# Optimization experiments

Hardware: AMD Instinct MI355X
Metric: run time of the kernel (lower is better)

Reference implementation:

```python
import jax, jax.numpy as jnp
import numpy as np

N = 10000      # num nodes
E = 320000     # num edges
IN = 256       # in_dim
MP = 256       # mp_width
FL = 512       # fl_width
OUT = 64       # out_dim


def setup_inputs() -> dict:
    key = jax.random.key(0)
    ks = jax.random.split(key, 20)
    inp = {}
    inp["x"] = jax.random.normal(ks[0], (N, IN), dtype=jnp.float32)
    inp["edge_index"] = jax.random.randint(ks[1], (2, E), 0, N, dtype=jnp.int64)
    # iMP (frozen) linear layers: weight ~ N(0, 1) per nn.init.normal_(std=1.0)
    inp["mp_w0"] = jax.random.normal(ks[2], (IN, MP), dtype=jnp.float32)
    inp["mp_b0"] = jax.random.uniform(ks[3], (MP,), minval=-1.0, maxval=1.0) / np.sqrt(IN)
    inp["mp_w1"] = jax.random.normal(ks[4], (MP, MP), dtype=jnp.float32)
    inp["mp_b1"] = jax.random.uniform(ks[5], (MP,), minval=-1.0, maxval=1.0) / np.sqrt(MP)
    inp["mp_w2"] = jax.random.normal(ks[6], (MP, MP), dtype=jnp.float32)
    inp["mp_b2"] = jax.random.uniform(ks[7], (MP,), minval=-1.0, maxval=1.0) / np.sqrt(MP)
    # FC layers (torch default Linear init scale ~ 1/sqrt(fan_in))
    inp["fc_w0"] = jax.random.normal(ks[8], (MP, FL), dtype=jnp.float32) / np.sqrt(MP)
    inp["fc_b0"] = jnp.zeros((FL,), dtype=jnp.float32)
    inp["fc_w1"] = jax.random.normal(ks[9], (FL, FL), dtype=jnp.float32) / np.sqrt(FL)
    inp["fc_b1"] = jnp.zeros((FL,), dtype=jnp.float32)
    # injection projections
    inp["inj_w0"] = jax.random.normal(ks[10], (MP, FL), dtype=jnp.float32) / np.sqrt(MP)
    inp["inj_b0"] = jnp.zeros((FL,), dtype=jnp.float32)
    inp["inj_w1"] = jax.random.normal(ks[11], (MP, FL), dtype=jnp.float32) / np.sqrt(MP)
    inp["inj_b1"] = jnp.zeros((FL,), dtype=jnp.float32)
    inp["alpha"] = jnp.array(1.0, dtype=jnp.float32)
    inp["out_w"] = jax.random.normal(ks[12], (FL, OUT), dtype=jnp.float32) / np.sqrt(FL)
    inp["out_b"] = jnp.zeros((OUT,), dtype=jnp.float32)
    return inp


def _imp(x, w, b, row, col, deg_inv):
    # h = relu(W x); h /= deg; Ah = scatter_add over row of h[col]
    h = jax.nn.relu(x @ w + b) * deg_inv[:, None]      # [N, out]
    return jnp.zeros_like(h).at[row].add(h[col])       # gather + scatter-add


def reference(x, edge_index, mp_w0, mp_b0, mp_w1, mp_b1, mp_w2, mp_b2,
              fc_w0, fc_b0, fc_w1, fc_b1, inj_w0, inj_b0, inj_w1, inj_b1,
              alpha, out_w, out_b):
    row, col = edge_index[0], edge_index[1]
    deg = jax.ops.segment_sum(jnp.ones((E,), x.dtype), col, num_segments=N)
    # nodes with deg==0 never appear in col so clamping does not change output
    deg_inv = 1.0 / jnp.maximum(deg, 1.0)

    h = _imp(x, mp_w0, mp_b0, row, col, deg_inv)
    h = _imp(h, mp_w1, mp_b1, row, col, deg_inv)
    h = _imp(h, mp_w2, mp_b2, row, col, deg_inv)

    x_inject = h
    h = alpha * (jax.nn.relu(h) @ fc_w0 + fc_b0) + (x_inject @ inj_w0 + inj_b0)
    h = alpha * (jax.nn.relu(h) @ fc_w1 + fc_b1) + (x_inject @ inj_w1 + inj_b1)
    return h @ out_w + out_b
```

## Files before the change

### kernel.cpp

```cpp
#include <hip/hip_runtime.h>

#define N_NODES 10000
#define N_EDGES 320000
#define MPAD 10112
#define NBIN 10048
#define CHUNK 2048
#define NCH 157
#define CAP 128
#define PREP_BLOCKS 512
#define PREP_TOT 1148480L

typedef unsigned short u16;
typedef short bf16x8 __attribute__((ext_vector_type(8)));
typedef float f32x4 __attribute__((ext_vector_type(4)));

__device__ __forceinline__ u16 f2b(float f) {
  unsigned u = __builtin_bit_cast(unsigned, f);
  unsigned r = u + 0x7fffu + ((u >> 16) & 1u);
  return (u16)(r >> 16);
}
__device__ __forceinline__ unsigned pack2(float a, float b) {
  return (unsigned)f2b(a) | ((unsigned)f2b(b) << 16);
}
__device__ __forceinline__ float blo(unsigned u) { return __builtin_bit_cast(float, u << 16); }
__device__ __forceinline__ float bhi(unsigned u) { return __builtin_bit_cast(float, u & 0xffff0000u); }

struct PP {
  const float *x;
  const float *w0, *w1, *w2, *fcw0, *injw0, *fcw1, *injw1, *outw;
  const float *fcb0, *injb0, *fcb1, *injb1, *alpha, *outb;
  u16 *xb, *w0t, *w1t, *w2t, *wc1t, *wft;
  float *bias1, *bf;
};

__global__ __launch_bounds__(256) void edge_hist(const int* __restrict__ ei,
                                                 unsigned* __restrict__ histRC) {
  __shared__ unsigned sh[NBIN];
  const int tid = threadIdx.x, ch = blockIdx.x;
  for (int i = tid; i < NBIN; i += 256) sh[i] = 0;
  __syncthreads();
  const int e0 = ch * CHUNK;
#pragma unroll
  for (int j = 0; j < CHUNK; j += 256) {
    int e = e0 + j + tid;
    if (e < N_EDGES) {
      atomicAdd(&sh[ei[e]], 1u);
      atomicAdd(&sh[ei[N_EDGES + e]], 65536u);
    }
  }
  __syncthreads();
  for (int i = tid; i < NBIN; i += 256)
    histRC[(size_t)ch * NBIN + i] = sh[i];
}

__global__ __launch_bounds__(256) void prep(PP P) {
  const float alpha = P.alpha[0];
  const long stride = (long)PREP_BLOCKS * 256;
  for (long ii = (long)blockIdx.x * 256 + threadIdx.x; ii < PREP_TOT; ii += stride) {
    long i = ii;
    if (i < 640000L) {
      float4 v = ((const float4*)P.x)[i];
      uint2 o;
      o.x = pack2(v.x, v.y);
      o.y = pack2(v.z, v.w);
      *(uint2*)(P.xb + 4 * i) = o;
      continue;
    }
    i -= 640000L;
    if (i < 65536) { P.w0t[i] = f2b(P.w0[(i & 255) * 256 + (i >> 8)]); continue; }
    i -= 65536;
    if (i < 65536) { P.w1t[i] = f2b(P.w1[(i & 255) * 256 + (i >> 8)]); continue; }
    i -= 65536;
    if (i < 65536) { P.w2t[i] = f2b(P.w2[(i & 255) * 256 + (i >> 8)]); continue; }
    i -= 65536;
    if (i < 262144) {
      int n = (int)(i >> 9), k = (int)(i & 511);
      float v = (k < 256) ? alpha * P.fcw0[k * 512 + n] : P.injw0[(k - 256) * 512 + n];
      P.wc1t[i] = f2b(v); continue;
    }
    i -= 262144;
    if (i < 49152) {
      int n = (int)(i & 63), k = (int)(i >> 6);
      const float* fr = (k < 512) ? P.fcw1 + (size_t)k * 512
                                  : P.injw1 + (size_t)(k - 512) * 512;
      float a0 = 0.f, a1 = 0.f, a2 = 0.f, a3 = 0.f;
#pragma unroll 4
      for (int j = 0; j < 512; j += 4) {
        float4 f = *(const float4*)(fr + j);
        a0 += f.x * P.outw[(j + 0) * 64 + n];
        a1 += f.y * P.outw[(j + 1) * 64 + n];
        a2 += f.z * P.outw[(j + 2) * 64 + n];
        a3 += f.w * P.outw[(j + 3) * 64 + n];
      }
      float acc = (a0 + a1) + (a2 + a3);
      if (k < 512) acc *= alpha;
      P.wft[n * 768 + k] = f2b(acc);
      continue;
    }
    i -= 49152;
    if (i < 64) {
      float acc = P.outb[i];
#pragma unroll 8
      for (int j = 0; j < 512; ++j)
        acc += (alpha * P.fcb1[j] + P.injb1[j]) * P.outw[j * 64 + i];
      P.bf[i] = acc;
      continue;
    }
    i -= 64;
    if (i < 512) { P.bias1[i] = alpha * P.fcb0[i] + P.injb0[i]; continue; }
  }
}

__global__ __launch_bounds__(64) void col_scan(const unsigned* __restrict__ histRC,
                                               u16* __restrict__ chunkoff,
                                               int* __restrict__ cnt,
                                               float* __restrict__ deg_inv) {
  int r = blockIdx.x * 64 + threadIdx.x;
  if (r >= MPAD) return;
  if (r >= NBIN) { deg_inv[r] = 1.0f; return; }
  unsigned run = 0;
#pragma unroll 8
  for (int ch = 0; ch < NCH; ++ch) {
    chunkoff[(size_t)ch * NBIN + r] = (u16)(run & 0xffffu);
    run += histRC[(size_t)ch * NBIN + r];
  }
  int cr = (int)(run & 0xffffu);
  int dg = (int)(run >> 16);
  cnt[r] = cr;
  deg_inv[r] = 1.0f / (float)(dg > 1 ? dg : 1);
}

__global__ __launch_bounds__(256) void place_edges(const int* __restrict__ ei,
                                                   const u16* __restrict__ chunkoff,
                                                   int* __restrict__ csr) {
  __shared__ int cur[NBIN];
  const int ch = blockIdx.x, t = threadIdx.x;
  const u16* co = chunkoff + (size_t)ch * NBIN;
  for (int i = t; i < NBIN; i += 256) cur[i] = co[i];
  __syncthreads();
  const int e0 = ch * CHUNK;
#pragma unroll
  for (int j = 0; j < CHUNK; j += 256) {
    int e = e0 + j + t;
    if (e < N_EDGES) {
      int r = ei[e];
      int c = ei[N_EDGES + e];
      int rank = atomicAdd(&cur[r], 1);
      if (rank < CAP) csr[r * CAP + rank] = c;
    }
  }
}

template<int K, bool RELU, bool SCALE, bool F32OUT>
__global__ __launch_bounds__(128) void gemm64(
    const u16* __restrict__ A, int lda,
    const u16* __restrict__ Bt,
    const float* __restrict__ bias,
    const float* __restrict__ scale,
    u16* __restrict__ Cb, float* __restrict__ Cf, int ldc)
{
  __shared__ u16 As[64 * 72];
  __shared__ u16 Bs[64 * 72];
  const int tid = threadIdx.x;
  const int m0 = blockIdx.x * 64;
  const int n0 = blockIdx.y * 64;
  const int wave = tid >> 6;
  const int lane = tid & 63;
  const int wr = wave * 32;
  const int lm = lane & 15;
  const int koff = (lane >> 4) * 8;

  const int srow = tid >> 2;
  const int scol = (tid & 3) * 16;
  const u16* Ag0 = A + (size_t)(m0 + srow) * lda + scol;
  const u16* Ag1 = A + (size_t)(m0 + srow + 32) * lda + scol;
  const u16* Bg0 = Bt + (size_t)(n0 + srow) * K + scol;
  const u16* Bg1 = Bt + (size_t)(n0 + srow + 32) * K + scol;
  u16* Asw0 = &As[srow * 72 + scol];
  u16* Asw1 = &As[(srow + 32) * 72 + scol];
  u16* Bsw0 = &Bs[srow * 72 + scol];
  u16* Bsw1 = &Bs[(srow + 32) * 72 + scol];

  f32x4 acc[2][4] = {};

  int4 pa0 = *(const int4*)(Ag0),     pa1 = *(const int4*)(Ag0 + 8);
  int4 pa2 = *(const int4*)(Ag1),     pa3 = *(const int4*)(Ag1 + 8);
  int4 pb0 = *(const int4*)(Bg0),     pb1 = *(const int4*)(Bg0 + 8);
  int4 pb2 = *(const int4*)(Bg1),     pb3 = *(const int4*)(Bg1 + 8);

#pragma unroll
  for (int kb = 0; kb < K; kb += 64) {
    __syncthreads();
    *(int4*)Asw0 = pa0; *(int4*)(Asw0 + 8) = pa1;
    *(int4*)Asw1 = pa2; *(int4*)(Asw1 + 8) = pa3;
    *(int4*)Bsw0 = pb0; *(int4*)(Bsw0 + 8) = pb1;
    *(int4*)Bsw1 = pb2; *(int4*)(Bsw1 + 8) = pb3;
    __syncthreads();
    if (kb + 64 < K) {
      pa0 = *(const int4*)(Ag0 + kb + 64); pa1 = *(const int4*)(Ag0 + kb + 72);
      pa2 = *(const int4*)(Ag1 + kb + 64); pa3 = *(const int4*)(Ag1 + kb + 72);
      pb0 = *(const int4*)(Bg0 + kb + 64); pb1 = *(const int4*)(Bg0 + kb + 72);
      pb2 = *(const int4*)(Bg1 + kb + 64); pb3 = *(const int4*)(Bg1 + kb + 72);
    }
#pragma unroll
    for (int ks = 0; ks < 2; ++ks) {
      bf16x8 af[2], bf[4];
#pragma unroll
      for (int mi = 0; mi < 2; ++mi)
        af[mi] = *(const bf16x8*)&As[(wr + mi * 16 + lm) * 72 + ks * 32 + koff];
#pragma unroll
      for (int ni = 0; ni < 4; ++ni)
        bf[ni] = *(const bf16x8*)&Bs[(ni * 16 + lm) * 72 + ks * 32 + koff];
#pragma unroll
      for (int mi = 0; mi < 2; ++mi)
#pragma unroll
        for (int ni = 0; ni < 4; ++ni)
          acc[mi][ni] = __builtin_amdgcn_mfma_f32_16x16x32_bf16(af[mi], bf[ni], acc[mi][ni], 0, 0, 0);
    }
  }

  const int q4 = (lane >> 4) * 4;
#pragma unroll
  for (int mi = 0; mi < 2; ++mi) {
#pragma unroll
    for (int ni = 0; ni < 4; ++ni) {
      const int gc = n0 + ni * 16 + lm;
      const float bv = bias[gc];
#pragma unroll
      for (int r = 0; r < 4; ++r) {
        const int gr = m0 + wr + mi * 16 + q4 + r;
        float v = acc[mi][ni][r] + bv;
        if (RELU) v = fmaxf(v, 0.f);
        if (SCALE) v *= scale[gr];
        if (F32OUT) {
          if (gr < N_NODES) Cf[(size_t)gr * ldc + gc] = v;
        } else {
          Cb[(size_t)gr * ldc + gc] = f2b(v);
        }
      }
    }
  }
}

__global__ __launch_bounds__(256) void aggregate(
    const u16* __restrict__ tmp, const int* __restrict__ cnt,
    const int* __restrict__ csr, u16* __restrict__ out0,
    u16* __restrict__ A1, u16* __restrict__ A2, int mode)
{
  const int wv = threadIdx.x >> 6;
  const int lane = threadIdx.x & 63;
  const int r = blockIdx.x * 4 + wv;
  const int half = lane >> 5;
  const int q = lane & 31;
  const int beg = r * CAP, end = beg + cnt[r];
  const size_t feat = (size_t)q * 16;
  const char* tb = (const char*)tmp;

  float s0 = 0.f, s1 = 0.f, s2 = 0.f, s3 = 0.f, s4 = 0.f, s5 = 0.f, s6 = 0.f, s7 = 0.f;
  int i = beg;
  for (; i + 16 <= end; i += 16) {
    uint4 v[8];
#pragma unroll
    for (int j = 0; j < 8; ++j)
      v[j] = *(const uint4*)(tb + (size_t)csr[i + 2 * j + half] * 512 + feat);
#pragma unroll
    for (int j = 0; j < 8; ++j) {
      s0 += blo(v[j].x); s1 += bhi(v[j].x); s2 += blo(v[j].y); s3 += bhi(v[j].y);
      s4 += blo(v[j].z); s5 += bhi(v[j].z); s6 += blo(v[j].w); s7 += bhi(v[j].w);
    }
  }
  for (; i + 8 <= end; i += 8) {
    uint4 v[4];
#pragma unroll
    for (int j = 0; j < 4; ++j)
      v[j] = *(const uint4*)(tb + (size_t)csr[i + 2 * j + half] * 512 + feat);
#pragma unroll
    for (int j = 0; j < 4; ++j) {
      s0 += blo(v[j].x); s1 += bhi(v[j].x); s2 += blo(v[j].y); s3 += bhi(v[j].y);
      s4 += blo(v[j].z); s5 += bhi(v[j].z); s6 += blo(v[j].w); s7 += bhi(v[j].w);
    }
  }
  for (; i < end; i += 2) {
    int id = i + half;
    if (id < end) {
      uint4 v = *(const uint4*)(tb + (size_t)csr[id] * 512 + feat);
      s0 += blo(v.x); s1 += bhi(v.x); s2 += blo(v.y); s3 += bhi(v.y);
      s4 += blo(v.z); s5 += bhi(v.z); s6 += blo(v.w); s7 += bhi(v.w);
    }
  }
  const int src = lane ^ 32;
  s0 += __shfl(s0, src, 64); s1 += __shfl(s1, src, 64);
  s2 += __shfl(s2, src, 64); s3 += __shfl(s3, src, 64);
  s4 += __shfl(s4, src, 64); s5 += __shfl(s5, src, 64);
  s6 += __shfl(s6, src, 64); s7 += __shfl(s7, src, 64);

  if (half == 0) {
    uint4 pv;
    pv.x = pack2(s0, s1); pv.y = pack2(s2, s3);
    pv.z = pack2(s4, s5); pv.w = pack2(s6, s7);
    if (mode == 0) {
      *(uint4*)((char*)out0 + (size_t)r * 512 + feat) = pv;
    } else {
      uint4 pr;
      pr.x = pack2(fmaxf(s0, 0.f), fmaxf(s1, 0.f));
      pr.y = pack2(fmaxf(s2, 0.f), fmaxf(s3, 0.f));
      pr.z = pack2(fmaxf(s4, 0.f), fmaxf(s5, 0.f));
      pr.w = pack2(fmaxf(s6, 0.f), fmaxf(s7, 0.f));
      *(uint4*)((char*)A1 + (size_t)r * 1024 + feat) = pr;
      *(uint4*)((char*)A1 + (size_t)r * 1024 + 512 + feat) = pv;
      *(uint4*)((char*)A2 + (size_t)r * 1536 + 1024 + feat) = pv;
    }
  }
}

extern "C" void kernel_launch(void* const* d_in, const int* in_sizes, int n_in,
                              void* d_out, int out_size, void* d_ws, size_t ws_size,
                              hipStream_t stream) {
  const int* ei = (const int*)d_in[1];

  char* p = (char*)d_ws;
  auto carve = [&](size_t bytes) -> void* {
    void* r = (void*)p;
    p += (bytes + 255) & ~(size_t)255;
    return r;
  };
  unsigned* histRC  = (unsigned*)carve((size_t)NCH * NBIN * 4);
  u16*    chunkoff  = (u16*)carve((size_t)NCH * NBIN * 2);
  int*    cnt       = (int*)carve(NBIN * 4);
  int*    csr       = (int*)carve((size_t)NBIN * CAP * 4);
  float*  deg_inv   = (float*)carve(MPAD * 4);
  float*  bias1     = (float*)carve(512 * 4);
  float*  bf        = (float*)carve(64 * 4);
  u16* xb   = (u16*)carve((size_t)MPAD * 256 * 2);
  u16* w0t  = (u16*)carve(65536 * 2);
  u16* w1t  = (u16*)carve(65536 * 2);
  u16* w2t  = (u16*)carve(65536 * 2);
  u16* wc1t = (u16*)carve(262144 * 2);
  u16* wft  = (u16*)carve(49152 * 2);
  u16* tmp  = (u16*)carve((size_t)MPAD * 256 * 2);
  u16* h    = (u16*)carve((size_t)MPAD * 256 * 2);
  u16* cat1 = (u16*)carve((size_t)MPAD * 512 * 2);
  u16* cat2 = (u16*)carve((size_t)MPAD * 768 * 2);

  PP pp;
  pp.x = (const float*)d_in[0];
  pp.w0 = (const float*)d_in[2];
  pp.w1 = (const float*)d_in[4];
  pp.w2 = (const float*)d_in[6];
  pp.fcw0 = (const float*)d_in[8];
  pp.fcw1 = (const float*)d_in[10];
  pp.injw0 = (const float*)d_in[12];
  pp.injw1 = (const float*)d_in[14];
  pp.outw = (const float*)d_in[17];
  pp.fcb0 = (const float*)d_in[9];
  pp.injb0 = (const float*)d_in[13];
  pp.fcb1 = (const float*)d_in[11];
  pp.injb1 = (const float*)d_in[15];
  pp.alpha = (const float*)d_in[16];
  pp.outb = (const float*)d_in[18];
  pp.xb = xb; pp.w0t = w0t; pp.w1t = w1t; pp.w2t = w2t;
  pp.wc1t = wc1t; pp.wft = wft;
  pp.bias1 = bias1; pp.bf = bf;

  const float* mp_b0 = (const float*)d_in[3];
  const float* mp_b1 = (const float*)d_in[5];
  const float* mp_b2 = (const float*)d_in[7];
  float* out = (float*)d_out;

  edge_hist<<<NCH, 256, 0, stream>>>(ei, histRC);
  prep<<<PREP_BLOCKS, 256, 0, stream>>>(pp);
  col_scan<<<MPAD / 64, 64, 0, stream>>>(histRC, chunkoff, cnt, deg_inv);
  place_edges<<<NCH, 256, 0, stream>>>(ei, chunkoff, csr);

  dim3 gmp(MPAD / 64, 4), gfc(MPAD / 64, 8), go(MPAD / 64, 1);
  gemm64<256, true, true, false><<<gmp, 128, 0, stream>>>(xb, 256, w0t, mp_b0, deg_inv, tmp, nullptr, 256);
  aggregate<<<2500, 256, 0, stream>>>(tmp, cnt, csr, h, nullptr, nullptr, 0);
  gemm64<256, true, true, false><<<gmp, 128, 0, stream>>>(h, 256, w1t, mp_b1, deg_inv, tmp, nullptr, 256);
  aggregate<<<2500, 256, 0, stream>>>(tmp, cnt, csr, h, nullptr, nullptr, 0);
  gemm64<256, true, true, false><<<gmp, 128, 0, stream>>>(h, 256, w2t, mp_b2, deg_inv, tmp, nullptr, 256);
  aggregate<<<2500, 256, 0, stream>>>(tmp, cnt, csr, nullptr, cat1, cat2, 1);
  gemm64<512, true, false, false><<<gfc, 128, 0, stream>>>(cat1, 512, wc1t, bias1, nullptr, cat2, nullptr, 768);
  gemm64<768, false, false, true><<<go, 128, 0, stream>>>(cat2, 768, wft, bf, nullptr, nullptr, out, 64);
}
```

Measured before the change: 250.5 us.

## Build CSR with global atomics fused into prep; drop concat buffer copy

Replaces the three-kernel CSR build (per-chunk histogram, column scan, placement) with global atomic cursor and degree counters, run inside the prep kernel by extra blocks, after a memset. Degree inverse is now computed inline in the GEMM epilogue. The final GEMM reads its A operand from two separate buffers, so the aggregate no longer writes a duplicate copy into a wide concat buffer. The aggregate's 16-wide unrolled loop is also removed. This cuts kernel launches and scan traffic, at the cost of contended global atomics and a nondeterministic neighbour order.

```diff
diff --git a/kernel.cpp b/kernel.cpp
--- a/kernel.cpp
+++ b/kernel.cpp
@@ -4,9 +4,8 @@
 #define N_EDGES 320000
 #define MPAD 10112
 #define NBIN 10048
-#define CHUNK 2048
-#define NCH 157
 #define CAP 128
+#define EBLKS 157
 #define PREP_BLOCKS 512
 #define PREP_TOT 1148480L
 
@@ -26,37 +25,36 @@
 __device__ __forceinline__ float bhi(unsigned u) { return __builtin_bit_cast(float, u & 0xffff0000u); }
 
 struct PP {
-  const float *x;
+  const float *x; const int *ei;
   const float *w0, *w1, *w2, *fcw0, *injw0, *fcw1, *injw1, *outw;
   const float *fcb0, *injb0, *fcb1, *injb1, *alpha, *outb;
   u16 *xb, *w0t, *w1t, *w2t, *wc1t, *wft;
   float *bias1, *bf;
+  int *cursor, *deg, *csr;
 };
 
-__global__ __launch_bounds__(256) void edge_hist(const int* __restrict__ ei,
-                                                 unsigned* __restrict__ histRC) {
-  __shared__ unsigned sh[NBIN];
-  const int tid = threadIdx.x, ch = blockIdx.x;
-  for (int i = tid; i < NBIN; i += 256) sh[i] = 0;
-  __syncthreads();
-  const int e0 = ch * CHUNK;
-#pragma unroll
-  for (int j = 0; j < CHUNK; j += 256) {
-    int e = e0 + j + tid;
-    if (e < N_EDGES) {
-      atomicAdd(&sh[ei[e]], 1u);
-      atomicAdd(&sh[ei[N_EDGES + e]], 65536u);
-    }
-  }
-  __syncthreads();
-  for (int i = tid; i < NBIN; i += 256)
-    histRC[(size_t)ch * NBIN + i] = sh[i];
-}
-
-__global__ __launch_bounds__(256) void prep(PP P) {
+__global__ __launch_bounds__(256) void prep_place(PP P) {
+  const int tid = threadIdx.x, bid = blockIdx.x;
+
+  if (bid < EBLKS) {
+    const int e0 = bid * 2048;
+#pragma unroll
+    for (int j = 0; j < 2048; j += 256) {
+      int e = e0 + j + tid;
+      if (e < N_EDGES) {
+        int r = P.ei[e];
+        int c = P.ei[N_EDGES + e];
+        int pos = atomicAdd(&P.cursor[r], 1);
+        if (pos < CAP) P.csr[r * CAP + pos] = c;
+        atomicAdd(&P.deg[c], 1);
+      }
+    }
+    return;
+  }
+
   const float alpha = P.alpha[0];
   const long stride = (long)PREP_BLOCKS * 256;
-  for (long ii = (long)blockIdx.x * 256 + threadIdx.x; ii < PREP_TOT; ii += stride) {
+  for (long ii = (long)(bid - EBLKS) * 256 + tid; ii < PREP_TOT; ii += stride) {
     long i = ii;
     if (i < 640000L) {
       float4 v = ((const float4*)P.x)[i];
@@ -111,52 +109,12 @@
   }
 }
 
-__global__ __launch_bounds__(64) void col_scan(const unsigned* __restrict__ histRC,
-                                               u16* __restrict__ chunkoff,
-                                               int* __restrict__ cnt,
-                                               float* __restrict__ deg_inv) {
-  int r = blockIdx.x * 64 + threadIdx.x;
-  if (r >= MPAD) return;
-  if (r >= NBIN) { deg_inv[r] = 1.0f; return; }
-  unsigned run = 0;
-#pragma unroll 8
-  for (int ch = 0; ch < NCH; ++ch) {
-    chunkoff[(size_t)ch * NBIN + r] = (u16)(run & 0xffffu);
-    run += histRC[(size_t)ch * NBIN + r];
-  }
-  int cr = (int)(run & 0xffffu);
-  int dg = (int)(run >> 16);
-  cnt[r] = cr;
-  deg_inv[r] = 1.0f / (float)(dg > 1 ? dg : 1);
-}
-
-__global__ __launch_bounds__(256) void place_edges(const int* __restrict__ ei,
-                                                   const u16* __restrict__ chunkoff,
-                                                   int* __restrict__ csr) {
-  __shared__ int cur[NBIN];
-  const int ch = blockIdx.x, t = threadIdx.x;
-  const u16* co = chunkoff + (size_t)ch * NBIN;
-  for (int i = t; i < NBIN; i += 256) cur[i] = co[i];
-  __syncthreads();
-  const int e0 = ch * CHUNK;
-#pragma unroll
-  for (int j = 0; j < CHUNK; j += 256) {
-    int e = e0 + j + t;
-    if (e < N_EDGES) {
-      int r = ei[e];
-      int c = ei[N_EDGES + e];
-      int rank = atomicAdd(&cur[r], 1);
-      if (rank < CAP) csr[r * CAP + rank] = c;
-    }
-  }
-}
-
 template<int K, bool RELU, bool SCALE, bool F32OUT>
 __global__ __launch_bounds__(128) void gemm64(
     const u16* __restrict__ A, int lda,
     const u16* __restrict__ Bt,
     const float* __restrict__ bias,
-    const float* __restrict__ scale,
+    const int* __restrict__ deg,
     u16* __restrict__ Cb, float* __restrict__ Cf, int ldc)
 {
   __shared__ u16 As[64 * 72];
@@ -231,7 +189,7 @@
         const int gr = m0 + wr + mi * 16 + q4 + r;
         float v = acc[mi][ni][r] + bv;
         if (RELU) v = fmaxf(v, 0.f);
-        if (SCALE) v *= scale[gr];
+        if (SCALE) v *= 1.0f / fmaxf((float)deg[gr], 1.0f);
         if (F32OUT) {
           if (gr < N_NODES) Cf[(size_t)gr * ldc + gc] = v;
         } else {
@@ -242,33 +200,115 @@
   }
 }
 
+__global__ __launch_bounds__(128) void gemm_fold(
+    const u16* __restrict__ Ar,
+    const u16* __restrict__ Ah,
+    const u16* __restrict__ Bt,
+    const float* __restrict__ bias,
+    float* __restrict__ Cf)
+{
+  const int K = 768;
+  __shared__ u16 As[64 * 72];
+  __shared__ u16 Bs[64 * 72];
+  const int tid = threadIdx.x;
+  const int m0 = blockIdx.x * 64;
+  const int n0 = 0;
+  const int wave = tid >> 6;
+  const int lane = tid & 63;
+  const int wr = wave * 32;
+  const int lm = lane & 15;
+  const int koff = (lane >> 4) * 8;
+
+  const int srow = tid >> 2;
+  const int scol = (tid & 3) * 16;
+  const int ar0 = m0 + srow, ar1 = m0 + srow + 32;
+  auto aptr = [&](int row, int col) -> const u16* {
+    return (col < 512) ? Ar + (size_t)row * 512 + col
+                       : Ah + (size_t)row * 512 + (col - 512);
+  };
+  const u16* Bg0 = Bt + (size_t)(n0 + srow) * K + scol;
+  const u16* Bg1 = Bt + (size_t)(n0 + srow + 32) * K + scol;
+  u16* Asw0 = &As[srow * 72 + scol];
+  u16* Asw1 = &As[(srow + 32) * 72 + scol];
+  u16* Bsw0 = &Bs[srow * 72 + scol];
+  u16* Bsw1 = &Bs[(srow + 32) * 72 + scol];
+
+  f32x4 acc[2][4] = {};
+
+  int4 pa0 = *(const int4*)aptr(ar0, scol);
+  int4 pa1 = *(const int4*)aptr(ar0, scol + 8);
+  int4 pa2 = *(const int4*)aptr(ar1, scol);
+  int4 pa3 = *(const int4*)aptr(ar1, scol + 8);
+  int4 pb0 = *(const int4*)(Bg0), pb1 = *(const int4*)(Bg0 + 8);
+  int4 pb2 = *(const int4*)(Bg1), pb3 = *(const int4*)(Bg1 + 8);
+
+#pragma unroll
+  for (int kb = 0; kb < K; kb += 64) {
+    __syncthreads();
+    *(int4*)Asw0 = pa0; *(int4*)(Asw0 + 8) = pa1;
+    *(int4*)Asw1 = pa2; *(int4*)(Asw1 + 8) = pa3;
+    *(int4*)Bsw0 = pb0; *(int4*)(Bsw0 + 8) = pb1;
+    *(int4*)Bsw1 = pb2; *(int4*)(Bsw1 + 8) = pb3;
+    __syncthreads();
+    if (kb + 64 < K) {
+      int c = kb + 64 + scol;
+      pa0 = *(const int4*)aptr(ar0, c);
+      pa1 = *(const int4*)aptr(ar0, c + 8);
+      pa2 = *(const int4*)aptr(ar1, c);
+      pa3 = *(const int4*)aptr(ar1, c + 8);
+      pb0 = *(const int4*)(Bg0 + kb + 64); pb1 = *(const int4*)(Bg0 + kb + 72);
+      pb2 = *(const int4*)(Bg1 + kb + 64); pb3 = *(const int4*)(Bg1 + kb + 72);
+    }
+#pragma unroll
+    for (int ks = 0; ks < 2; ++ks) {
+      bf16x8 af[2], bf[4];
+#pragma unroll
+      for (int mi = 0; mi < 2; ++mi)
+        af[mi] = *(const bf16x8*)&As[(wr + mi * 16 + lm) * 72 + ks * 32 + koff];
+#pragma unroll
+      for (int ni = 0; ni < 4; ++ni)
+        bf[ni] = *(const bf16x8*)&Bs[(ni * 16 + lm) * 72 + ks * 32 + koff];
+#pragma unroll
+      for (int mi = 0; mi < 2; ++mi)
+#pragma unroll
+        for (int ni = 0; ni < 4; ++ni)
+          acc[mi][ni] = __builtin_amdgcn_mfma_f32_16x16x32_bf16(af[mi], bf[ni], acc[mi][ni], 0, 0, 0);
+    }
+  }
+
+  const int q4 = (lane >> 4) * 4;
+#pragma unroll
+  for (int mi = 0; mi < 2; ++mi) {
+#pragma unroll
+    for (int ni = 0; ni < 4; ++ni) {
+      const int gc = ni * 16 + lm;
+      const float bv = bias[gc];
+#pragma unroll
+      for (int r = 0; r < 4; ++r) {
+        const int gr = m0 + wr + mi * 16 + q4 + r;
+        if (gr < N_NODES) Cf[(size_t)gr * 64 + gc] = acc[mi][ni][r] + bv;
+      }
+    }
+  }
+}
+
 __global__ __launch_bounds__(256) void aggregate(
     const u16* __restrict__ tmp, const int* __restrict__ cnt,
     const int* __restrict__ csr, u16* __restrict__ out0,
-    u16* __restrict__ A1, u16* __restrict__ A2, int mode)
+    u16* __restrict__ A1, int mode)
 {
   const int wv = threadIdx.x >> 6;
   const int lane = threadIdx.x & 63;
   const int r = blockIdx.x * 4 + wv;
   const int half = lane >> 5;
   const int q = lane & 31;
-  const int beg = r * CAP, end = beg + cnt[r];
+  int n = cnt[r]; if (n > CAP) n = CAP;
+  const int beg = r * CAP, end = beg + n;
   const size_t feat = (size_t)q * 16;
   const char* tb = (const char*)tmp;
 
   float s0 = 0.f, s1 = 0.f, s2 = 0.f, s3 = 0.f, s4 = 0.f, s5 = 0.f, s6 = 0.f, s7 = 0.f;
   int i = beg;
-  for (; i + 16 <= end; i += 16) {
-    uint4 v[8];
-#pragma unroll
-    for (int j = 0; j < 8; ++j)
-      v[j] = *(const uint4*)(tb + (size_t)csr[i + 2 * j + half] * 512 + feat);
-#pragma unroll
-    for (int j = 0; j < 8; ++j) {
-      s0 += blo(v[j].x); s1 += bhi(v[j].x); s2 += blo(v[j].y); s3 += bhi(v[j].y);
-      s4 += blo(v[j].z); s5 += bhi(v[j].z); s6 += blo(v[j].w); s7 += bhi(v[j].w);
-    }
-  }
   for (; i + 8 <= end; i += 8) {
     uint4 v[4];
 #pragma unroll
@@ -308,7 +348,6 @@
       pr.w = pack2(fmaxf(s6, 0.f), fmaxf(s7, 0.f));
       *(uint4*)((char*)A1 + (size_t)r * 1024 + feat) = pr;
       *(uint4*)((char*)A1 + (size_t)r * 1024 + 512 + feat) = pv;
-      *(uint4*)((char*)A2 + (size_t)r * 1536 + 1024 + feat) = pv;
     }
   }
 }
@@ -324,26 +363,25 @@
     p += (bytes + 255) & ~(size_t)255;
     return r;
   };
-  unsigned* histRC  = (unsigned*)carve((size_t)NCH * NBIN * 4);
-  u16*    chunkoff  = (u16*)carve((size_t)NCH * NBIN * 2);
-  int*    cnt       = (int*)carve(NBIN * 4);
-  int*    csr       = (int*)carve((size_t)NBIN * CAP * 4);
-  float*  deg_inv   = (float*)carve(MPAD * 4);
-  float*  bias1     = (float*)carve(512 * 4);
-  float*  bf        = (float*)carve(64 * 4);
-  u16* xb   = (u16*)carve((size_t)MPAD * 256 * 2);
-  u16* w0t  = (u16*)carve(65536 * 2);
-  u16* w1t  = (u16*)carve(65536 * 2);
-  u16* w2t  = (u16*)carve(65536 * 2);
-  u16* wc1t = (u16*)carve(262144 * 2);
-  u16* wft  = (u16*)carve(49152 * 2);
-  u16* tmp  = (u16*)carve((size_t)MPAD * 256 * 2);
-  u16* h    = (u16*)carve((size_t)MPAD * 256 * 2);
-  u16* cat1 = (u16*)carve((size_t)MPAD * 512 * 2);
-  u16* cat2 = (u16*)carve((size_t)MPAD * 768 * 2);
+  int*   deg     = (int*)carve(MPAD * 4);
+  int*   cursor  = (int*)carve(NBIN * 4);
+  int*   csr     = (int*)carve((size_t)NBIN * CAP * 4);
+  float* bias1   = (float*)carve(512 * 4);
+  float* bf      = (float*)carve(64 * 4);
+  u16* xb    = (u16*)carve((size_t)MPAD * 256 * 2);
+  u16* w0t   = (u16*)carve(65536 * 2);
+  u16* w1t   = (u16*)carve(65536 * 2);
+  u16* w2t   = (u16*)carve(65536 * 2);
+  u16* wc1t  = (u16*)carve(262144 * 2);
+  u16* wft   = (u16*)carve(49152 * 2);
+  u16* tmp   = (u16*)carve((size_t)MPAD * 256 * 2);
+  u16* h     = (u16*)carve((size_t)MPAD * 256 * 2);
+  u16* cat1  = (u16*)carve((size_t)MPAD * 512 * 2);
+  u16* relu1 = (u16*)carve((size_t)MPAD * 512 * 2);
 
   PP pp;
   pp.x = (const float*)d_in[0];
+  pp.ei = ei;
   pp.w0 = (const float*)d_in[2];
   pp.w1 = (const float*)d_in[4];
   pp.w2 = (const float*)d_in[6];
@@ -361,24 +399,23 @@
   pp.xb = xb; pp.w0t = w0t; pp.w1t = w1t; pp.w2t = w2t;
   pp.wc1t = wc1t; pp.wft = wft;
   pp.bias1 = bias1; pp.bf = bf;
+  pp.cursor = cursor; pp.deg = deg; pp.csr = csr;
 
   const float* mp_b0 = (const float*)d_in[3];
   const float* mp_b1 = (const float*)d_in[5];
   const float* mp_b2 = (const float*)d_in[7];
   float* out = (float*)d_out;
 
-  edge_hist<<<NCH, 256, 0, stream>>>(ei, histRC);
-  prep<<<PREP_BLOCKS, 256, 0, stream>>>(pp);
-  col_scan<<<MPAD / 64, 64, 0, stream>>>(histRC, chunkoff, cnt, deg_inv);
-  place_edges<<<NCH, 256, 0, stream>>>(ei, chunkoff, csr);
+  hipMemsetAsync(deg, 0, (size_t)(MPAD + NBIN) * 4, stream);
+  prep_place<<<EBLKS + PREP_BLOCKS, 256, 0, stream>>>(pp);
 
   dim3 gmp(MPAD / 64, 4), gfc(MPAD / 64, 8), go(MPAD / 64, 1);
-  gemm64<256, true, true, false><<<gmp, 128, 0, stream>>>(xb, 256, w0t, mp_b0, deg_inv, tmp, nullptr, 256);
-  aggregate<<<2500, 256, 0, stream>>>(tmp, cnt, csr, h, nullptr, nullptr, 0);
-  gemm64<256, true, true, false><<<gmp, 128, 0, stream>>>(h, 256, w1t, mp_b1, deg_inv, tmp, nullptr, 256);
-  aggregate<<<2500, 256, 0, stream>>>(tmp, cnt, csr, h, nullptr, nullptr, 0);
-  gemm64<256, true, true, false><<<gmp, 128, 0, stream>>>(h, 256, w2t, mp_b2, deg_inv, tmp, nullptr, 256);
-  aggregate<<<2500, 256, 0, stream>>>(tmp, cnt, csr, nullptr, cat1, cat2, 1);
-  gemm64<512, true, false, false><<<gfc, 128, 0, stream>>>(cat1, 512, wc1t, bias1, nullptr, cat2, nullptr, 768);
-  gemm64<768, false, false, true><<<go, 128, 0, stream>>>(cat2, 768, wft, bf, nullptr, nullptr, out, 64);
-}
+  gemm64<256, true, true, false><<<gmp, 128, 0, stream>>>(xb, 256, w0t, mp_b0, deg, tmp, nullptr, 256);
+  aggregate<<<2500, 256, 0, stream>>>(tmp, cursor, csr, h, nullptr, 0);
+  gemm64<256, true, true, false><<<gmp, 128, 0, stream>>>(h, 256, w1t, mp_b1, deg, tmp, nullptr, 256);
+  aggregate<<<2500, 256, 0, stream>>>(tmp, cursor, csr, h, nullptr, 0);
+  gemm64<256, true, true, false><<<gmp, 128, 0, stream>>>(h, 256, w2t, mp_b2, deg, tmp, nullptr, 256);
+  aggregate<<<2500, 256, 0, stream>>>(tmp, cursor, csr, nullptr, cat1, 1);
+  gemm64<512, true, false, false><<<gfc, 128, 0, stream>>>(cat1, 512, wc1t, bias1, nullptr, relu1, nullptr, 512);
+  gemm_fold<<<go, 128, 0, stream>>>(relu1, cat1 + 256, wft, bf, out);
+}
```

Measured after the change: 234.3 us. 6.5% less time.
